# Optimization experiments

Hardware: AMD Instinct MI355X
Metric: run time of the kernel (lower is better)

## Reference

```python
import jax, jax.numpy as jnp
import numpy as np

B, S, D, H = 2, 2048, 2048, 16
HD = D // H  # 128


def _rope_tables(seq_len, half_dim, theta=10000.0):
    freqs = 1.0 / (theta ** (np.arange(0, half_dim, dtype=np.float32) / half_dim))
    t = np.arange(seq_len, dtype=np.float32)
    ang = np.outer(t, freqs)  # [S, HD//2]
    return jnp.asarray(np.cos(ang)), jnp.asarray(np.sin(ang))


def setup_inputs() -> dict:
    key = jax.random.key(0)
    kx, kq, kk, kv, ko = jax.random.split(key, 5)
    cos, sin = _rope_tables(S, HD // 2)
    return {
        "x": jax.random.normal(kx, (B, S, D), dtype=jnp.float32),
        "cos": cos,  # [S, HD//2]
        "sin": sin,  # [S, HD//2]
        "wq": jax.random.normal(kq, (D, D), dtype=jnp.float32) * 0.02,
        "wk": jax.random.normal(kk, (D, D), dtype=jnp.float32) * 0.02,
        "wv": jax.random.normal(kv, (D, D), dtype=jnp.float32) * 0.02,
        "wo": jax.random.normal(ko, (D, D), dtype=jnp.float32) * 0.02,
    }


def _apply_rotary(t, cos, sin):
    # t: [B, S, H, HD]; rotate consecutive pairs (complex multiply)
    t2 = t.reshape(*t.shape[:-1], HD // 2, 2)
    te, to = t2[..., 0], t2[..., 1]
    c = cos[None, :, None, :]
    s = sin[None, :, None, :]
    out = jnp.stack([te * c - to * s, te * s + to * c], axis=-1)
    return out.reshape(t.shape)


def reference(x, cos, sin, wq, wk, wv, wo):
    xq = (x @ wq).reshape(B, S, H, HD)
    xk = (x @ wk).reshape(B, S, H, HD)
    xv = (x @ wv).reshape(B, S, H, HD)
    # FAITHFUL to source: rotary applied to xq and xv (NOT xk)
    xq = _apply_rotary(xq, cos, sin)
    xv = _apply_rotary(xv, cos, sin)
    q = xq.transpose(0, 2, 1, 3)  # [B,H,S,HD]
    k = xk.transpose(0, 2, 1, 3)
    v = xv.transpose(0, 2, 1, 3)
    scores = jnp.einsum("bhqd,bhkd->bhqk", q, k) / jnp.sqrt(jnp.float32(HD))
    mask = jnp.triu(jnp.full((S, S), -jnp.inf, dtype=scores.dtype), k=1)
    scores = scores + mask[None, None, :, :]
    probs = jax.nn.softmax(scores, axis=-1)
    out = jnp.einsum("bhqk,bhkd->bhqd", probs, v)  # [B,H,S,HD]
    out = out.transpose(0, 2, 1, 3).reshape(B, S, D)
    return out @ wo
```

## Files before the change

### kernel.cpp

```cpp
#include <hip/hip_runtime.h>
#include <hip/hip_bf16.h>

typedef short short8 __attribute__((ext_vector_type(8)));
typedef float f32x4 __attribute__((ext_vector_type(4)));
typedef int int4v __attribute__((ext_vector_type(4)));

#define B_ 2
#define S_ 2048
#define D_ 2048
#define H_ 16
#define HD_ 128
#define K_ 2048

#define GLL16(gp, lp) __builtin_amdgcn_global_load_lds( \
    (const __attribute__((address_space(1))) void*)(gp), \
    (__attribute__((address_space(3))) void*)(lp), 16, 0, 0)

__device__ inline ushort f2bf(float f) {
    union { float f; unsigned u; } v; v.f = f;
    unsigned r = v.u + 0x7FFFu + ((v.u >> 16) & 1u);
    return (ushort)(r >> 16);
}
__device__ inline float bf2f(ushort b) {
    union { unsigned u; float f; } v; v.u = ((unsigned)b) << 16;
    return v.f;
}

__device__ inline short8 rope8(short8 raw, const float* __restrict__ cosp,
                               const float* __restrict__ sinp) {
    float4 cs = *reinterpret_cast<const float4*>(cosp);
    float4 sn = *reinterpret_cast<const float4*>(sinp);
    const float* c = reinterpret_cast<const float*>(&cs);
    const float* s = reinterpret_cast<const float*>(&sn);
    short8 out;
    #pragma unroll
    for (int j = 0; j < 4; ++j) {
        float a = bf2f((ushort)raw[2 * j]), b = bf2f((ushort)raw[2 * j + 1]);
        out[2 * j]     = (short)f2bf(fmaf(a, c[j], -(b * s[j])));
        out[2 * j + 1] = (short)f2bf(fmaf(a, s[j], b * c[j]));
    }
    return out;
}

__global__ __launch_bounds__(256) void prep_kernel(
        const float* __restrict__ s0, const float* __restrict__ s1,
        const float* __restrict__ s2, const float* __restrict__ s3,
        ushort* __restrict__ d0, ushort* __restrict__ d1,
        ushort* __restrict__ d2, ushort* __restrict__ d3,
        const float* __restrict__ x, ushort* __restrict__ xb) {
    const int z = blockIdx.z;
    const int t = threadIdx.x;
    if (z >= 4) {
        const int lane = (((z - 4) * 1024 + blockIdx.y * 32 + blockIdx.x) << 8) + t;
        #pragma unroll
        for (int k = 0; k < 4; ++k) {
            int i = lane + k * 524288;
            float4 v = reinterpret_cast<const float4*>(x)[i];
            ushort4 o;
            o.x = f2bf(v.x); o.y = f2bf(v.y); o.z = f2bf(v.z); o.w = f2bf(v.w);
            reinterpret_cast<ushort4*>(xb)[i] = o;
        }
        return;
    }
    __shared__ ushort tile[64][72];
    const float* src = (z == 0) ? s0 : (z == 1) ? s1 : (z == 2) ? s2 : s3;
    ushort* dst = (z == 0) ? d0 : (z == 1) ? d1 : (z == 2) ? d2 : d3;
    const int bk = blockIdx.y * 64, bn = blockIdx.x * 64;
    #pragma unroll
    for (int it = 0; it < 4; ++it) {
        int id = t + it * 256;
        int row = id >> 4;
        int c4 = (id & 15) * 4;
        float4 v = *reinterpret_cast<const float4*>(&src[(size_t)(bk + row) * D_ + bn + c4]);
        ushort4 o; o.x = f2bf(v.x); o.y = f2bf(v.y); o.z = f2bf(v.z); o.w = f2bf(v.w);
        *reinterpret_cast<ushort4*>(&tile[row][c4]) = o;
    }
    __syncthreads();
    #pragma unroll
    for (int it = 0; it < 4; ++it) {
        int id = t + it * 256;
        int n = id >> 4;
        int c4 = (id & 15) * 4;
        ushort4 o;
        o.x = tile[c4 + 0][n]; o.y = tile[c4 + 1][n];
        o.z = tile[c4 + 2][n]; o.w = tile[c4 + 3][n];
        *reinterpret_cast<ushort4*>(&dst[(size_t)(bn + n) * D_ + bk + c4]) = o;
    }
}

#define BAR8() __builtin_amdgcn_s_barrier()
#define VMC0() asm volatile("s_waitcnt vmcnt(0)" ::: "memory")

template<int MODE>
__global__ __launch_bounds__(512, 2) void gemm8(const ushort* __restrict__ A,
        const ushort* __restrict__ Bt, ushort* __restrict__ q0, ushort* __restrict__ k0,
        ushort* __restrict__ v0, float* __restrict__ outf,
        const float* __restrict__ cosT, const float* __restrict__ sinT, int nbx) {
    constexpr int NC      = (MODE == 0) ? 3 : 4;
    constexpr int NF      = (MODE == 0) ? 4 : 2;
    constexpr int ACCR    = NF * 2;
    constexpr int BN      = (MODE == 0) ? 192 : 128;
    constexpr int NBCH    = BN / 64;
    constexpr int WCOLS   = (MODE == 0) ? 48 : 64;
    constexpr int BBYTES  = BN * 128;
    constexpr int BSTRIDE = 32768 + BBYTES;

    extern __shared__ char smem[];
    const int tid = threadIdx.x, lane = tid & 63, wv = tid >> 6;
    const int wm = (MODE == 0) ? (wv >> 2) : (wv >> 1);
    const int wn = (MODE == 0) ? (wv & 3) : (wv & 1);
    const int l15 = lane & 15, lg = lane >> 4;
    const int nwg = (int)gridDim.x, cpx = nwg >> 3;
    const int swzb = ((int)blockIdx.x & 7) * cpx + ((int)blockIdx.x >> 3);
    const int bn = (swzb % nbx) * BN, bm = (swzb / nbx) * 256;

    f32x4 acc[ACCR][NC] = {};

    const int grl = wv * 8 + (lane >> 3);
    const int swc = (((lane & 7) ^ ((lane >> 3) & 7)) * 8);
    const ushort* Ag = A + (size_t)(bm + grl) * K_ + swc;
    const ushort* Bg = Bt + (size_t)(bn + grl) * K_ + swc;
    const size_t rowHA = (size_t)128 * K_;
    const size_t row64 = (size_t)64 * K_;

#define VMCN() do { if (MODE == 0) asm volatile("s_waitcnt vmcnt(3)" ::: "memory"); \
                    else           asm volatile("s_waitcnt vmcnt(2)" ::: "memory"); } while (0)
#define STAGE_A(t, h) do { if ((t) < 32) { \
        const ushort* g = Ag + (size_t)(h) * rowHA + (size_t)(t) * 64; \
        char* l = smem + (((t) & 1) ? BSTRIDE : 0) + ((h) << 14) + (wv << 10); \
        GLL16(g, l); GLL16(g + row64, l + 8192); } } while (0)
#define STAGE_B(t, ch) do { if ((t) < 32) { \
        const ushort* g = Bg + (size_t)(ch) * row64 + (size_t)(t) * 64; \
        char* l = smem + (((t) & 1) ? BSTRIDE : 0) + 32768 + (ch) * 8192 + (wv << 10); \
        GLL16(g, l); } } while (0)
#define STAGE_B_ALL(t) do { _Pragma("unroll") \
        for (int ch = 0; ch < NBCH; ++ch) STAGE_B(t, ch); } while (0)

    const int colsw0 = (lg * 16) ^ ((l15 & 7) << 4);
    const int colsw1 = (64 + lg * 16) ^ ((l15 & 7) << 4);
    const char* abase0 = smem + wm * (NF * 4096);
    const char* bbase0 = smem + 32768;
    const char* abase1 = abase0 + BSTRIDE;
    const char* bbase1 = bbase0 + BSTRIDE;

#define LDA(ab, q, cs) do { _Pragma("unroll") for (int f = 0; f < NF; ++f) \
        a[f] = *reinterpret_cast<const short8*>((ab) + ((q) * (NF * 16) + f * 16 + l15) * 128 + (cs)); } while (0)
#define LDB(bb, cs) do { _Pragma("unroll") for (int c = 0; c < NC; ++c) { \
        const int rw = wn * WCOLS + c * 16; \
        b[c] = *reinterpret_cast<const short8*>((bb) + (rw >> 6) * 8192 + ((rw & 63) + l15) * 128 + (cs)); } } while (0)
#define MM(q) do { __builtin_amdgcn_s_setprio(1); \
        _Pragma("unroll") for (int f = 0; f < NF; ++f) \
        _Pragma("unroll") for (int c = 0; c < NC; ++c) \
            acc[(q) * NF + f][c] = __builtin_amdgcn_mfma_f32_16x16x32_bf16(a[f], b[c], acc[(q) * NF + f][c], 0, 0, 0); \
        __builtin_amdgcn_s_setprio(0); } while (0)

    STAGE_A(0, 0); STAGE_A(0, 1);
    STAGE_B_ALL(0);
    STAGE_B_ALL(1);
    VMCN();
    BAR8();

    for (int i = 0; i < 16; ++i) {
        const int t1 = 2 * i + 1, s0 = 2 * i + 2, s1 = 2 * i + 3;
        short8 a[NF], b[NC];
        LDB(bbase0, colsw0); LDA(abase0, 0, colsw0);
        STAGE_A(t1, 0);
        BAR8(); MM(0); BAR8();
        LDA(abase0, 1, colsw0);
        STAGE_A(t1, 1);
        BAR8(); MM(1); BAR8();
        LDB(bbase0, colsw1); LDA(abase0, 0, colsw1);
        BAR8(); MM(0); BAR8();
        LDA(abase0, 1, colsw1);
        STAGE_B_ALL(s0);
        if (s0 < 32) VMCN(); else VMC0();
        BAR8(); MM(1); BAR8();
        LDB(bbase1, colsw0); LDA(abase1, 0, colsw0);
        STAGE_A(s0, 0);
        BAR8(); MM(0); BAR8();
        LDA(abase1, 1, colsw0);
        STAGE_A(s0, 1);
        BAR8(); MM(1); BAR8();
        LDB(bbase1, colsw1); LDA(abase1, 0, colsw1);
        BAR8(); MM(0); BAR8();
        LDA(abase1, 1, colsw1);
        STAGE_B_ALL(s1);
        if (s1 < 32) VMCN(); else VMC0();
        BAR8(); MM(1); BAR8();
    }

    if (MODE == 0) {
        ushort* eb = (ushort*)smem;
        #pragma unroll
        for (int c = 0; c < NC; ++c)
            #pragma unroll
            for (int rf = 0; rf < ACCR; ++rf)
                #pragma unroll
                for (int j = 0; j < 4; ++j) {
                    int r = wm * 128 + rf * 16 + lg * 4 + j;
                    int cl = wn * WCOLS + c * 16 + l15;
                    eb[r * 216 + cl] = f2bf(acc[rf][c][j]);
                }
        __syncthreads();
        const int rql = lane >> 2;
        const int cgrp = lane & 3;
        #pragma unroll
        for (int p = 0; p < 2; ++p) {
            const int row = p * 128 + wv * 16 + rql;
            const int grow = bm + row;
            const int bb = grow >> 11, s = grow & (S_ - 1);
            const float* cr = cosT + (size_t)s * 64;
            const float* sr = sinT + (size_t)s * 64;
            const ushort* ebr = eb + row * 216;
            #pragma unroll
            for (int t = 0; t < 6; ++t) {
                const int coln = (cgrp + t * 4) * 8;
                const int colg = bn + coln;
                const int seg = colg >> 11;
                const int h = (colg >> 7) & (H_ - 1), d = colg & (HD_ - 1);
                short8 v8 = *reinterpret_cast<const short8*>(ebr + coln);
                if (seg != 1)
                    v8 = rope8(v8, cr + (d >> 1), sr + (d >> 1));
                ushort* segp = (seg == 0) ? q0 : ((seg == 1) ? k0 : v0);
                *reinterpret_cast<short8*>(segp + (((size_t)(bb * H_ + h)) * S_ + s) * HD_ + d) = v8;
            }
        }
    } else {
        #pragma unroll
        for (int rf = 0; rf < ACCR; ++rf)
            #pragma unroll
            for (int c = 0; c < NC; ++c)
                #pragma unroll
                for (int j = 0; j < 4; ++j) {
                    int row = bm + wm * (NF * 32) + rf * 16 + lg * 4 + j;
                    int col = bn + wn * WCOLS + c * 16 + l15;
                    outf[(size_t)row * D_ + col] = acc[rf][c][j];
                }
    }
#undef VMCN
#undef STAGE_A
#undef STAGE_B
#undef STAGE_B_ALL
#undef LDA
#undef LDB
#undef MM
}

__global__ __launch_bounds__(512, 4) void attn5(const ushort* __restrict__ Qm,
        const ushort* __restrict__ Km, const ushort* __restrict__ Vm,
        ushort* __restrict__ Om) {
    __shared__ __align__(16) ushort Kb[2][64 * 128];
    __shared__ __align__(16) ushort Vt[2][128][72];
    const int tid = threadIdx.x, lane = tid & 63, wv = tid >> 6;
    const int l15 = lane & 15, lg = lane >> 4;
    const int yy = (int)blockIdx.y;
    const int qt = (yy < 8) ? (15 - 2 * yy) : (2 * (yy - 8));
    const int bh = blockIdx.x;
    const size_t base = (size_t)bh * S_ * HD_;
    const int qrow0 = qt * 128 + wv * 16;
    const float C = 0.1275174f;

    short8 qf[4];
    {
        const ushort* qp = Qm + base + (size_t)(qrow0 + l15) * HD_;
        #pragma unroll
        for (int c = 0; c < 4; ++c)
            qf[c] = *reinterpret_cast<const short8*>(qp + c * 32 + lg * 8);
    }
    f32x4 oacc[8] = {};
    float mS = -1e30f, lS = 0.f;
    const int ntiles = 2 * qt + 2;
    const int kmask0 = 2 * qt + (wv >> 2);

    {
        #pragma unroll
        for (int c = 0; c < 2; ++c) {
            int row = wv * 8 + c * 4 + (lane >> 4);
            GLL16(Km + base + (size_t)row * HD_ + (((lane & 15) ^ (row & 7)) << 3),
                  &Kb[0][wv * 1024 + c * 512]);
        }
        const ushort* vp = Vm + base + (size_t)lane * HD_ + wv * 16;
        #pragma unroll
        for (int cc = 0; cc < 2; ++cc) {
            int4v v = *reinterpret_cast<const int4v*>(vp + cc * 8);
            const ushort* e = reinterpret_cast<const ushort*>(&v);
            #pragma unroll
            for (int j = 0; j < 8; ++j) Vt[0][wv * 16 + cc * 8 + j][lane] = e[j];
        }
    }
    __syncthreads();

    int cur = 0;
    for (int kt = 0; kt < ntiles; ++kt) {
        const bool pfn = (kt + 1 < ntiles);
        int4v vr[2];
        if (pfn) {
            const int r0 = (kt + 1) * 64;
            #pragma unroll
            for (int c = 0; c < 2; ++c) {
                int row = wv * 8 + c * 4 + (lane >> 4);
                GLL16(Km + base + (size_t)(r0 + row) * HD_ + (((lane & 15) ^ (row & 7)) << 3),
                      &Kb[cur ^ 1][wv * 1024 + c * 512]);
            }
            const ushort* vp = Vm + base + (size_t)(r0 + lane) * HD_ + wv * 16;
            #pragma unroll
            for (int cc = 0; cc < 2; ++cc)
                vr[cc] = *reinterpret_cast<const int4v*>(vp + cc * 8);
        }
        f32x4 sacc[4] = {};
        const ushort* Kc = &Kb[cur][0];
        __builtin_amdgcn_s_setprio(1);
        #pragma unroll
        for (int ct = 0; ct < 4; ++ct) {
            const int row = ct * 16 + l15;
            const int sw = (row & 7) << 3;
            #pragma unroll
            for (int c = 0; c < 4; ++c) {
                short8 kf = *reinterpret_cast<const short8*>(
                    Kc + row * 128 + ((c * 32 + lg * 8) ^ sw));
                sacc[ct] = __builtin_amdgcn_mfma_f32_16x16x32_bf16(kf, qf[c], sacc[ct], 0, 0, 0);
            }
        }
        __builtin_amdgcn_s_setprio(0);

        float t16[16];
        #pragma unroll
        for (int ct = 0; ct < 4; ++ct)
            #pragma unroll
            for (int j = 0; j < 4; ++j) t16[ct * 4 + j] = sacc[ct][j];
        if (kt >= kmask0) {
            const int thr = qrow0 + l15 - kt * 64;
            #pragma unroll
            for (int ct = 0; ct < 4; ++ct)
                #pragma unroll
                for (int j = 0; j < 4; ++j)
                    if (ct * 16 + lg * 4 + j > thr) t16[ct * 4 + j] = -1e30f;
        }
        float mx[8];
        #pragma unroll
        for (int i = 0; i < 8; ++i) mx[i] = fmaxf(t16[i], t16[i + 8]);
        #pragma unroll
        for (int i = 0; i < 4; ++i) mx[i] = fmaxf(mx[i], mx[i + 4]);
        float m64 = fmaxf(fmaxf(mx[0], mx[1]), fmaxf(mx[2], mx[3]));
        m64 = fmaxf(m64, __shfl_xor(m64, 16));
        m64 = fmaxf(m64, __shfl_xor(m64, 32));
        if (!__all(m64 - mS <= 47.0f)) {
            float mnew = fmaxf(mS, m64);
            float corr = __builtin_amdgcn_exp2f((mS - mnew) * C);
            lS *= corr;
            #pragma unroll
            for (int dt = 0; dt < 8; ++dt)
                #pragma unroll
                for (int j = 0; j < 4; ++j) oacc[dt][j] *= corr;
            mS = mnew;
        }
        const float mcc = mS * C;
        float p[16];
        #pragma unroll
        for (int i = 0; i < 16; ++i)
            p[i] = __builtin_amdgcn_exp2f(fmaf(t16[i], C, -mcc));
        float sm[8];
        #pragma unroll
        for (int i = 0; i < 8; ++i) sm[i] = p[i] + p[i + 8];
        #pragma unroll
        for (int i = 0; i < 4; ++i) sm[i] = sm[i] + sm[i + 4];
        float psum = (sm[0] + sm[1]) + (sm[2] + sm[3]);
        psum += __shfl_xor(psum, 16);
        psum += __shfl_xor(psum, 32);
        lS += psum;

        unsigned dw[8];
        #pragma unroll
        for (int ct = 0; ct < 4; ++ct)
            #pragma unroll
            for (int u = 0; u < 2; ++u) {
                __hip_bfloat162 h2 = __float22bfloat162_rn(
                    float2{p[ct * 4 + 2 * u], p[ct * 4 + 2 * u + 1]});
                dw[ct * 2 + u] = *reinterpret_cast<unsigned*>(&h2);
            }
        #pragma unroll
        for (int c2 = 0; c2 < 2; ++c2) {
            int4v pfd;
            #pragma unroll
            for (int d = 0; d < 4; ++d) {
                int srcl = (lg & 1) * 32 + (d >> 1) * 16 + l15;
                int r0 = __shfl((int)dw[(2 * c2) * 2 + (d & 1)], srcl);
                int r1 = __shfl((int)dw[(2 * c2 + 1) * 2 + (d & 1)], srcl);
                pfd[d] = (lg & 2) ? r1 : r0;
            }
            short8 pf = *reinterpret_cast<short8*>(&pfd);
            __builtin_amdgcn_s_setprio(1);
            #pragma unroll
            for (int dt = 0; dt < 8; ++dt) {
                short8 vf = *reinterpret_cast<const short8*>(
                    &Vt[cur][dt * 16 + l15][c2 * 32 + lg * 8]);
                oacc[dt] = __builtin_amdgcn_mfma_f32_16x16x32_bf16(vf, pf, oacc[dt], 0, 0, 0);
            }
            __builtin_amdgcn_s_setprio(0);
        }
        if (pfn) {
            #pragma unroll
            for (int cc = 0; cc < 2; ++cc) {
                const ushort* e = reinterpret_cast<const ushort*>(&vr[cc]);
                #pragma unroll
                for (int j = 0; j < 8; ++j) Vt[cur ^ 1][wv * 16 + cc * 8 + j][lane] = e[j];
            }
        }
        __syncthreads();
        cur ^= 1;
    }
    const int b = bh >> 4, h = bh & (H_ - 1);
    const int q = qrow0 + l15;
    const float inv = 1.0f / lS;
    ushort* op = Om + ((size_t)(b * S_ + q)) * D_ + h * HD_;
    #pragma unroll
    for (int dt = 0; dt < 8; ++dt) {
        ushort4 o;
        o.x = f2bf(oacc[dt][0] * inv);
        o.y = f2bf(oacc[dt][1] * inv);
        o.z = f2bf(oacc[dt][2] * inv);
        o.w = f2bf(oacc[dt][3] * inv);
        *reinterpret_cast<ushort4*>(op + dt * 16 + lg * 4) = o;
    }
}

extern "C" void kernel_launch(void* const* d_in, const int* in_sizes, int n_in,
                              void* d_out, int out_size, void* d_ws, size_t ws_size,
                              hipStream_t stream) {
    const float* x    = (const float*)d_in[0];
    const float* cosT = (const float*)d_in[1];
    const float* sinT = (const float*)d_in[2];
    const float* wq   = (const float*)d_in[3];
    const float* wk   = (const float*)d_in[4];
    const float* wv   = (const float*)d_in[5];
    const float* wo   = (const float*)d_in[6];
    float* out = (float*)d_out;

    char* ws = (char*)d_ws;
    const size_t szX = (size_t)B_ * S_ * D_ * 2;
    const size_t szW = (size_t)D_ * D_ * 2;
    ushort* xb   = (ushort*)(ws);
    ushort* wcat = (ushort*)(ws + szX);
    ushort* woT  = (ushort*)(ws + szX + 3 * szW);
    ushort* q0   = (ushort*)(ws + szX + 4 * szW);
    ushort* k0   = (ushort*)(ws + szX + 4 * szW + szX);
    ushort* v0   = (ushort*)(ws + szX + 4 * szW + 2 * szX);
    ushort* att  = xb;

    hipFuncSetAttribute(reinterpret_cast<const void*>(&gemm8<0>),
                        hipFuncAttributeMaxDynamicSharedMemorySize, 114688);
    hipFuncSetAttribute(reinterpret_cast<const void*>(&gemm8<1>),
                        hipFuncAttributeMaxDynamicSharedMemorySize, 98304);

    prep_kernel<<<dim3(D_ / 64, D_ / 64, 6), 256, 0, stream>>>(
        wq, wk, wv, wo, wcat, wcat + (size_t)D_ * D_, wcat + 2 * (size_t)D_ * D_, woT,
        x, xb);

    gemm8<0><<<512, 512, 114688, stream>>>(xb, wcat, q0, k0, v0, nullptr, cosT, sinT, 32);

    attn5<<<dim3(B_ * H_, S_ / 128), 512, 0, stream>>>(q0, k0, v0, att);

    gemm8<1><<<256, 512, 98304, stream>>>(att, woT, nullptr, nullptr, nullptr, out,
                                          nullptr, nullptr, 16);
}
```

Measured before the change: 244.0 us.

## Split QKV GEMM into dedicated 256x384-tile kernel with 12 waves

Replaces the templated QKV GEMM with a dedicated kernel using 768 threads, 256x384 output tiles, 256 workgroups and 160KB LDS. Loads are split by wave role: four waves stage A, six stage B, and all twelve run MFMA. The epilogue writes each half of the tile through LDS before applying rope. The larger tile is meant to raise arithmetic intensity and cut global reloads of A and B, at the cost of fewer workgroups, one workgroup per CU given the LDS size, and more barriers.

```diff
diff --git a/kernel.cpp b/kernel.cpp
--- a/kernel.cpp
+++ b/kernel.cpp
@@ -90,29 +90,143 @@
 
 #define BAR8() __builtin_amdgcn_s_barrier()
 #define VMC0() asm volatile("s_waitcnt vmcnt(0)" ::: "memory")
-
-template<int MODE>
-__global__ __launch_bounds__(512, 2) void gemm8(const ushort* __restrict__ A,
+#define VMC8() asm volatile("s_waitcnt vmcnt(8)" ::: "memory")
+
+__global__ __launch_bounds__(768, 3) void gemmQKV(const ushort* __restrict__ A,
         const ushort* __restrict__ Bt, ushort* __restrict__ q0, ushort* __restrict__ k0,
-        ushort* __restrict__ v0, float* __restrict__ outf,
-        const float* __restrict__ cosT, const float* __restrict__ sinT, int nbx) {
-    constexpr int NC      = (MODE == 0) ? 3 : 4;
-    constexpr int NF      = (MODE == 0) ? 4 : 2;
-    constexpr int ACCR    = NF * 2;
-    constexpr int BN      = (MODE == 0) ? 192 : 128;
-    constexpr int NBCH    = BN / 64;
-    constexpr int WCOLS   = (MODE == 0) ? 48 : 64;
-    constexpr int BBYTES  = BN * 128;
-    constexpr int BSTRIDE = 32768 + BBYTES;
-
+        ushort* __restrict__ v0, const float* __restrict__ cosT,
+        const float* __restrict__ sinT) {
     extern __shared__ char smem[];
     const int tid = threadIdx.x, lane = tid & 63, wv = tid >> 6;
-    const int wm = (MODE == 0) ? (wv >> 2) : (wv >> 1);
-    const int wn = (MODE == 0) ? (wv & 3) : (wv & 1);
+    const int wm = wv / 6, wn = wv % 6;
+    const int l15 = lane & 15, lg = lane >> 4;
+    const int swzb = ((int)blockIdx.x & 7) * 32 + ((int)blockIdx.x >> 3);
+    const int bn = (swzb & 15) * 384, bm = (swzb >> 4) * 256;
+
+    f32x4 acc[8][4] = {};
+
+    const int srow = lane >> 3;
+    const int swc = ((lane & 7) ^ srow) * 8;
+    const bool isA = (wv < 4), isB = (wv >= 4 && wv < 10);
+    const ushort* Sg = isA ? (A + (size_t)(bm + wv * 64 + srow) * K_ + swc)
+                           : (Bt + (size_t)(bn + (wv - 4) * 64 + srow) * K_ + swc);
+    const int aoff = wv * 8192;
+    const int boff = (wv - 4) * 8192;
+    const size_t row8 = (size_t)8 * K_;
+
+#define STGA(t) do { if (isA && (t) < 32) { \
+        char* l0 = smem + (((t) & 1) ? 32768 : 0) + aoff; \
+        const ushort* g0 = Sg + (size_t)(t) * 64; \
+        _Pragma("unroll") for (int g = 0; g < 8; ++g) GLL16(g0 + g * row8, l0 + g * 1024); } } while (0)
+#define STGB(t) do { if (isB && (t) < 32) { \
+        char* l0 = smem + 65536 + (((t) & 1) ? 49152 : 0) + boff; \
+        const ushort* g0 = Sg + (size_t)(t) * 64; \
+        _Pragma("unroll") for (int g = 0; g < 8; ++g) GLL16(g0 + g * row8, l0 + g * 1024); } } while (0)
+
+    const int colsw0 = (lg * 16) ^ ((l15 & 7) << 4);
+    const int colsw1 = (64 + lg * 16) ^ ((l15 & 7) << 4);
+    const char* ae = smem + wm * 16384;
+    const char* ao = ae + 32768;
+    const char* be = smem + 65536 + wn * 8192;
+    const char* bo = be + 49152;
+
+#define LDA(ab, q, cs) do { _Pragma("unroll") for (int f = 0; f < 4; ++f) \
+        a[f] = *reinterpret_cast<const short8*>((ab) + (q) * 8192 + (f * 16 + l15) * 128 + (cs)); } while (0)
+#define LDB(bb, cs) do { _Pragma("unroll") for (int c = 0; c < 4; ++c) \
+        b[c] = *reinterpret_cast<const short8*>((bb) + (c * 16 + l15) * 128 + (cs)); } while (0)
+#define MM(q) do { __builtin_amdgcn_s_setprio(1); \
+        _Pragma("unroll") for (int f = 0; f < 4; ++f) \
+        _Pragma("unroll") for (int c = 0; c < 4; ++c) \
+            acc[(q) * 4 + f][c] = __builtin_amdgcn_mfma_f32_16x16x32_bf16(a[f], b[c], acc[(q) * 4 + f][c], 0, 0, 0); \
+        __builtin_amdgcn_s_setprio(0); } while (0)
+
+    STGA(0); STGB(0);
+    STGB(1);
+    if (wv < 4) VMC0(); else if (wv < 10) VMC8();
+    BAR8();
+
+    for (int i = 0; i < 16; ++i) {
+        const int t1 = 2 * i + 1, s0 = 2 * i + 2, s1 = 2 * i + 3;
+        short8 a[4], b[4];
+        LDB(be, colsw0); LDA(ae, 0, colsw0);
+        STGA(t1);
+        BAR8(); MM(0); BAR8();
+        LDA(ae, 1, colsw0);
+        BAR8(); MM(1); BAR8();
+        LDB(be, colsw1); LDA(ae, 0, colsw1);
+        BAR8(); MM(0); BAR8();
+        LDA(ae, 1, colsw1);
+        STGB(s0);
+        if (wv < 4) { VMC0(); } else if (wv < 10) { if (s0 < 32) VMC8(); else VMC0(); }
+        BAR8(); MM(1); BAR8();
+        LDB(bo, colsw0); LDA(ao, 0, colsw0);
+        STGA(s0);
+        BAR8(); MM(0); BAR8();
+        LDA(ao, 1, colsw0);
+        BAR8(); MM(1); BAR8();
+        LDB(bo, colsw1); LDA(ao, 0, colsw1);
+        BAR8(); MM(0); BAR8();
+        LDA(ao, 1, colsw1);
+        STGB(s1);
+        if (wv < 4) { VMC0(); } else if (wv < 10) { if (s1 < 32) VMC8(); else VMC0(); }
+        BAR8(); MM(1); BAR8();
+    }
+
+    ushort* eb = (ushort*)smem;
+    #pragma unroll
+    for (int p = 0; p < 2; ++p) {
+        __syncthreads();
+        if (wm == p) {
+            #pragma unroll
+            for (int c = 0; c < 4; ++c)
+                #pragma unroll
+                for (int rf = 0; rf < 8; ++rf)
+                    #pragma unroll
+                    for (int j = 0; j < 4; ++j) {
+                        int r = rf * 16 + lg * 4 + j;
+                        int cl = wn * 64 + c * 16 + l15;
+                        eb[r * 392 + cl] = f2bf(acc[rf][c][j]);
+                    }
+        }
+        __syncthreads();
+        const int row = tid / 6, t6 = tid - row * 6;
+        const int grow = bm + p * 128 + row;
+        const int bb = grow >> 11, s = grow & (S_ - 1);
+        const float* cr = cosT + (size_t)s * 64;
+        const float* sr = sinT + (size_t)s * 64;
+        const ushort* ebr = eb + row * 392;
+        #pragma unroll
+        for (int cc = 0; cc < 8; ++cc) {
+            const int coln = (t6 + cc * 6) * 8;
+            const int colg = bn + coln;
+            const int seg = colg >> 11;
+            const int h = (colg >> 7) & (H_ - 1), d = colg & (HD_ - 1);
+            short8 v8 = *reinterpret_cast<const short8*>(ebr + coln);
+            if (seg != 1)
+                v8 = rope8(v8, cr + (d >> 1), sr + (d >> 1));
+            ushort* segp = (seg == 0) ? q0 : ((seg == 1) ? k0 : v0);
+            *reinterpret_cast<short8*>(segp + (((size_t)(bb * H_ + h)) * S_ + s) * HD_ + d) = v8;
+        }
+    }
+#undef STGA
+#undef STGB
+#undef LDA
+#undef LDB
+#undef MM
+}
+
+__global__ __launch_bounds__(512, 2) void gemmOut(const ushort* __restrict__ A,
+        const ushort* __restrict__ Bt, float* __restrict__ outf, int nbx) {
+    constexpr int NC = 4, NF = 2, ACCR = 4, NBCH = 2, WCOLS = 64;
+    constexpr int BBYTES = 128 * 128, BSTRIDE = 32768 + BBYTES;
+
+    extern __shared__ char smem[];
+    const int tid = threadIdx.x, lane = tid & 63, wv = tid >> 6;
+    const int wm = wv >> 1, wn = wv & 1;
     const int l15 = lane & 15, lg = lane >> 4;
     const int nwg = (int)gridDim.x, cpx = nwg >> 3;
     const int swzb = ((int)blockIdx.x & 7) * cpx + ((int)blockIdx.x >> 3);
-    const int bn = (swzb % nbx) * BN, bm = (swzb / nbx) * 256;
+    const int bn = (swzb % nbx) * 128, bm = (swzb / nbx) * 256;
 
     f32x4 acc[ACCR][NC] = {};
 
@@ -123,8 +237,7 @@
     const size_t rowHA = (size_t)128 * K_;
     const size_t row64 = (size_t)64 * K_;
 
-#define VMCN() do { if (MODE == 0) asm volatile("s_waitcnt vmcnt(3)" ::: "memory"); \
-                    else           asm volatile("s_waitcnt vmcnt(2)" ::: "memory"); } while (0)
+#define VMCN() asm volatile("s_waitcnt vmcnt(2)" ::: "memory")
 #define STAGE_A(t, h) do { if ((t) < 32) { \
         const ushort* g = Ag + (size_t)(h) * rowHA + (size_t)(t) * 64; \
         char* l = smem + (((t) & 1) ? BSTRIDE : 0) + ((h) << 14) + (wv << 10); \
@@ -189,54 +302,16 @@
         BAR8(); MM(1); BAR8();
     }
 
-    if (MODE == 0) {
-        ushort* eb = (ushort*)smem;
+    #pragma unroll
+    for (int rf = 0; rf < ACCR; ++rf)
         #pragma unroll
         for (int c = 0; c < NC; ++c)
             #pragma unroll
-            for (int rf = 0; rf < ACCR; ++rf)
-                #pragma unroll
-                for (int j = 0; j < 4; ++j) {
-                    int r = wm * 128 + rf * 16 + lg * 4 + j;
-                    int cl = wn * WCOLS + c * 16 + l15;
-                    eb[r * 216 + cl] = f2bf(acc[rf][c][j]);
-                }
-        __syncthreads();
-        const int rql = lane >> 2;
-        const int cgrp = lane & 3;
-        #pragma unroll
-        for (int p = 0; p < 2; ++p) {
-            const int row = p * 128 + wv * 16 + rql;
-            const int grow = bm + row;
-            const int bb = grow >> 11, s = grow & (S_ - 1);
-            const float* cr = cosT + (size_t)s * 64;
-            const float* sr = sinT + (size_t)s * 64;
-            const ushort* ebr = eb + row * 216;
-            #pragma unroll
-            for (int t = 0; t < 6; ++t) {
-                const int coln = (cgrp + t * 4) * 8;
-                const int colg = bn + coln;
-                const int seg = colg >> 11;
-                const int h = (colg >> 7) & (H_ - 1), d = colg & (HD_ - 1);
-                short8 v8 = *reinterpret_cast<const short8*>(ebr + coln);
-                if (seg != 1)
-                    v8 = rope8(v8, cr + (d >> 1), sr + (d >> 1));
-                ushort* segp = (seg == 0) ? q0 : ((seg == 1) ? k0 : v0);
-                *reinterpret_cast<short8*>(segp + (((size_t)(bb * H_ + h)) * S_ + s) * HD_ + d) = v8;
-            }
-        }
-    } else {
-        #pragma unroll
-        for (int rf = 0; rf < ACCR; ++rf)
-            #pragma unroll
-            for (int c = 0; c < NC; ++c)
-                #pragma unroll
-                for (int j = 0; j < 4; ++j) {
-                    int row = bm + wm * (NF * 32) + rf * 16 + lg * 4 + j;
-                    int col = bn + wn * WCOLS + c * 16 + l15;
-                    outf[(size_t)row * D_ + col] = acc[rf][c][j];
-                }
-    }
+            for (int j = 0; j < 4; ++j) {
+                int row = bm + wm * (NF * 32) + rf * 16 + lg * 4 + j;
+                int col = bn + wn * WCOLS + c * 16 + l15;
+                outf[(size_t)row * D_ + col] = acc[rf][c][j];
+            }
 #undef VMCN
 #undef STAGE_A
 #undef STAGE_B
@@ -447,19 +522,18 @@
     ushort* v0   = (ushort*)(ws + szX + 4 * szW + 2 * szX);
     ushort* att  = xb;
 
-    hipFuncSetAttribute(reinterpret_cast<const void*>(&gemm8<0>),
-                        hipFuncAttributeMaxDynamicSharedMemorySize, 114688);
-    hipFuncSetAttribute(reinterpret_cast<const void*>(&gemm8<1>),
+    hipFuncSetAttribute(reinterpret_cast<const void*>(&gemmQKV),
+                        hipFuncAttributeMaxDynamicSharedMemorySize, 163840);
+    hipFuncSetAttribute(reinterpret_cast<const void*>(&gemmOut),
                         hipFuncAttributeMaxDynamicSharedMemorySize, 98304);
 
     prep_kernel<<<dim3(D_ / 64, D_ / 64, 6), 256, 0, stream>>>(
         wq, wk, wv, wo, wcat, wcat + (size_t)D_ * D_, wcat + 2 * (size_t)D_ * D_, woT,
         x, xb);
 
-    gemm8<0><<<512, 512, 114688, stream>>>(xb, wcat, q0, k0, v0, nullptr, cosT, sinT, 32);
+    gemmQKV<<<256, 768, 163840, stream>>>(xb, wcat, q0, k0, v0, cosT, sinT);
 
     attn5<<<dim3(B_ * H_, S_ / 128), 512, 0, stream>>>(q0, k0, v0, att);
 
-    gemm8<1><<<256, 512, 98304, stream>>>(att, woT, nullptr, nullptr, nullptr, out,
-                                          nullptr, nullptr, 16);
-}
+    gemmOut<<<256, 512, 98304, stream>>>(att, woT, out, 16);
+}
```

New measurement: 677.8 us. 178% more time.
